# Performance work log

Measured on AMD Instinct MI355X. Metric: run time of the kernel, lower is better.

The kernel has to match this reference:

```python
import jax, jax.numpy as jnp
import numpy as np

TOP_K = 4
NORM_TOPK_PROB = True


def setup_inputs() -> dict:
    key = jax.random.key(0)
    kx, kg, k1, k3, k2 = jax.random.split(key, 5)
    B, S, H, I, E = 1, 2048, 1024, 512, 16
    scale = 0.02
    return {
        "hidden_states": jax.random.normal(kx, (B, S, H), jnp.float32),
        "gate_w": jax.random.normal(kg, (E, H), jnp.float32) * scale,   # router Linear weight [E,H]
        "w1": jax.random.normal(k1, (E, I, H), jnp.float32) * scale,    # intermediateDense per expert
        "w3": jax.random.normal(k3, (E, I, H), jnp.float32) * scale,    # intermediateDense2 per expert
        "w2": jax.random.normal(k2, (E, H, I), jnp.float32) * scale,    # outputDense per expert
    }


def reference(hidden_states, gate_w, w1, w3, w2):
    B, S, H = hidden_states.shape
    x = hidden_states.reshape(-1, H)                    # [T,H]
    T = x.shape[0]
    E = gate_w.shape[0]

    # Router: softmax in fp32, top-k, optional renorm (norm_topk_prob=True)
    router_logits = x @ gate_w.T                        # [T,E]
    probs = jax.nn.softmax(router_logits.astype(jnp.float32), axis=-1)
    routing_weights, selected = jax.lax.top_k(probs, TOP_K)   # [T,K], [T,K]
    if NORM_TOPK_PROB:
        routing_weights = routing_weights / routing_weights.sum(-1, keepdims=True)
    routing_weights = routing_weights.astype(x.dtype)

    # Dense per-token expert-weight matrix: zero for unselected experts, so
    # the combine below computes exactly the torch gather->FFN->index_add math.
    w = jnp.zeros((T, E), x.dtype).at[jnp.arange(T)[:, None], selected].add(routing_weights)

    # Gated SiLU FFN for every expert, combined with routing weights.
    h1 = jnp.einsum('th,eih->tei', x, w1)               # [T,E,I]
    h3 = jnp.einsum('th,eih->tei', x, w3)               # [T,E,I]
    act = jax.nn.silu(h1) * h3                          # [T,E,I]
    out = jnp.einsum('tei,ehi,te->th', act, w2, w)      # [T,H]
    return out.reshape(B, S, H)
```

## Files before the change

### kernel.cpp

```cpp
#include <hip/hip_runtime.h>
#include <hip/hip_bf16.h>

#define T 2048
#define H 1024
#define IDIM 512
#define E 16
#define TOPK 4
#define NPAIR (T * TOPK)

typedef short bf16x8 __attribute__((ext_vector_type(8)));
typedef float f32x4 __attribute__((ext_vector_type(4)));
typedef unsigned short u16x8 __attribute__((ext_vector_type(8)));

static __device__ __forceinline__ unsigned short f2bf(float f) {
    union { float f; unsigned int u; } v; v.f = f;
    unsigned int r = (v.u + 0x7FFFu + ((v.u >> 16) & 1u)) >> 16;
    return (unsigned short)r;
}
static __device__ __forceinline__ float bf2f(unsigned short s) {
    union { unsigned int u; float f; } v; v.u = ((unsigned int)s) << 16;
    return v.f;
}

static __device__ __forceinline__ void async_ld16(const unsigned short* g, unsigned short* l) {
    __builtin_amdgcn_global_load_lds((const __attribute__((address_space(1))) void*)g,
                                     (__attribute__((address_space(3))) void*)l, 16, 0, 0);
}

__global__ __launch_bounds__(256) void cvt3_kernel(
    const float* __restrict__ w1, const float* __restrict__ w3, const float* __restrict__ w2,
    unsigned short* __restrict__ d1, unsigned short* __restrict__ d3, unsigned short* __restrict__ d2)
{
    const int n8 = (E * IDIM * H) / 8;
    int region = blockIdx.x >> 11;
    int bid = blockIdx.x & 2047;
    const float* src = (region == 0) ? w1 : (region == 1) ? w3 : w2;
    unsigned short* dst = (region == 0) ? d1 : (region == 1) ? d3 : d2;
    int i = bid * 256 + threadIdx.x;
    const int stride = 2048 * 256;
#pragma unroll 2
    for (; i < n8; i += stride) {
        float4 a = ((const float4*)src)[2 * i];
        float4 b = ((const float4*)src)[2 * i + 1];
        u16x8 o;
        o[0] = f2bf(a.x); o[1] = f2bf(a.y); o[2] = f2bf(a.z); o[3] = f2bf(a.w);
        o[4] = f2bf(b.x); o[5] = f2bf(b.y); o[6] = f2bf(b.z); o[7] = f2bf(b.w);
        ((u16x8*)dst)[i] = o;
    }
}

__global__ __launch_bounds__(256) void router_kernel(
    const float* __restrict__ x, const float* __restrict__ gw,
    int* __restrict__ topk_idx, float* __restrict__ topk_w,
    unsigned short* __restrict__ xb)
{
    int tok = blockIdx.x * 4 + (threadIdx.x >> 6);
    int lane = threadIdx.x & 63;
    if (tok >= T) return;
    const float4* xt4 = (const float4*)(x + (size_t)tok * H);
    float4 xr[4];
#pragma unroll
    for (int j = 0; j < 4; ++j) xr[j] = xt4[lane + j * 64];
    ushort4* xbt = (ushort4*)(xb + (size_t)tok * H);
#pragma unroll
    for (int j = 0; j < 4; ++j) {
        ushort4 o;
        o.x = f2bf(xr[j].x); o.y = f2bf(xr[j].y);
        o.z = f2bf(xr[j].z); o.w = f2bf(xr[j].w);
        xbt[lane + j * 64] = o;
    }
    float logits[E];
#pragma unroll
    for (int e = 0; e < E; ++e) {
        const float4* ge4 = (const float4*)(gw + (size_t)e * H);
        float acc = 0.f;
#pragma unroll
        for (int j = 0; j < 4; ++j) {
            float4 g = ge4[lane + j * 64];
            acc += xr[j].x * g.x + xr[j].y * g.y + xr[j].z * g.z + xr[j].w * g.w;
        }
#pragma unroll
        for (int off = 32; off; off >>= 1) acc += __shfl_xor(acc, off, 64);
        logits[e] = acc;
    }
    if (lane == 0) {
        float m = logits[0];
#pragma unroll
        for (int e = 1; e < E; ++e) m = fmaxf(m, logits[e]);
        float p[E];
#pragma unroll
        for (int e = 0; e < E; ++e) p[e] = __expf(logits[e] - m);
        int sel[TOPK]; float wv[TOPK]; float tot = 0.f;
#pragma unroll
        for (int k = 0; k < TOPK; ++k) {
            int best = 0; float bv = -1.f;
#pragma unroll
            for (int e = 0; e < E; ++e) { if (p[e] > bv) { bv = p[e]; best = e; } }
            sel[k] = best; wv[k] = bv; tot += bv; p[best] = -2.f;
        }
#pragma unroll
        for (int k = 0; k < TOPK; ++k) {
            topk_idx[tok * TOPK + k] = sel[k];
            topk_w[tok * TOPK + k] = wv[k] / tot;
        }
    }
}

__global__ __launch_bounds__(1024) void route_build_kernel(
    const int* __restrict__ topk_idx, int* __restrict__ offsets,
    int* __restrict__ pair_token, int* __restrict__ inv_pos)
{
    __shared__ int h[E];
    __shared__ int cur[E];
    int tid = threadIdx.x;
    if (tid < E) h[tid] = 0;
    __syncthreads();
    int eloc[8];
#pragma unroll
    for (int j = 0; j < 8; ++j) {
        eloc[j] = topk_idx[tid * 8 + j];
        atomicAdd(&h[eloc[j]], 1);
    }
    __syncthreads();
    if (tid == 0) {
        int s = 0;
#pragma unroll
        for (int e = 0; e < E; ++e) { offsets[e] = s; cur[e] = s; s += h[e]; }
        offsets[E] = s;
    }
    __syncthreads();
#pragma unroll
    for (int j = 0; j < 8; ++j) {
        int i = tid * 8 + j;
        int pos = atomicAdd(&cur[eloc[j]], 1);
        pair_token[pos] = i >> 2;
        inv_pos[i] = pos;
    }
}


__global__ __launch_bounds__(256, 5) void gemm_a_kernel(
    const unsigned short* __restrict__ xb,
    const unsigned short* __restrict__ wb1,
    const unsigned short* __restrict__ wb3,
    const int* __restrict__ offsets,
    const int* __restrict__ pair_token,
    unsigned short* __restrict__ act)
{
    __shared__ unsigned short Xs[2][128 * 32];
    __shared__ unsigned short W1s[2][64 * 32];
    __shared__ unsigned short W3s[2][64 * 32];

    int bid = blockIdx.x;
    int xcd = bid & 7, s0 = bid >> 3;
    int yz = xcd * 16 + (s0 >> 4);
    int e = yz >> 3;
    int n0 = (yz & 7) * 64;
    int t0 = (s0 & 15) * 128;

    int beg = offsets[e];
    int cnt = offsets[e + 1] - beg;
    if (t0 >= cnt) return;

    int tid = threadIdx.x;
    int wave = tid >> 6, lane = tid & 63;

    const unsigned short* xg[2];
#pragma unroll
    for (int i = 0; i < 2; ++i) {
        int slot = wave * 128 + i * 64 + lane;
        int g = slot >> 3, sp = (slot & 7) ^ (g & 7);
        int row = g * 2 + (sp >> 2), c = sp & 3;
        int r = t0 + row; if (r >= cnt) r = cnt - 1;
        xg[i] = xb + (size_t)pair_token[beg + r] * H + c * 8;
    }
    const unsigned short* w1g;
    const unsigned short* w3g;
    {
        int slot = wave * 64 + lane;
        int g = slot >> 3, sp = (slot & 7) ^ (g & 7);
        int row = g * 2 + (sp >> 2), c = sp & 3;
        size_t off = (size_t)e * IDIM * H + (size_t)(n0 + row) * H + c * 8;
        w1g = wb1 + off;
        w3g = wb3 + off;
    }

    int wr = wave >> 1, wc = wave & 1;
    int lm = lane & 15, lq = lane >> 4;

    f32x4 acc1[4][2], acc3[4][2];
#pragma unroll
    for (int mi = 0; mi < 4; ++mi)
#pragma unroll
        for (int nj = 0; nj < 2; ++nj) {
            acc1[mi][nj] = (f32x4){0.f, 0.f, 0.f, 0.f};
            acc3[mi][nj] = (f32x4){0.f, 0.f, 0.f, 0.f};
        }

    int aoff[4], boff[2];
#pragma unroll
    for (int mi = 0; mi < 4; ++mi) {
        int m = wr * 64 + mi * 16 + lm;
        int g = m >> 1;
        aoff[mi] = g * 64 + (((lq + ((m & 1) << 2)) ^ (g & 7)) << 3);
    }
#pragma unroll
    for (int nj = 0; nj < 2; ++nj) {
        int n = wc * 32 + nj * 16 + lm;
        int g = n >> 1;
        boff[nj] = g * 64 + (((lq + ((n & 1) << 2)) ^ (g & 7)) << 3);
    }

#pragma unroll
    for (int i = 0; i < 2; ++i) async_ld16(xg[i], &Xs[0][(wave * 128 + i * 64) * 8]);
    async_ld16(w1g, &W1s[0][wave * 512]);
    async_ld16(w3g, &W3s[0][wave * 512]);

    const int NK = H / 32;
    for (int kk = 0; kk < NK; ++kk) {
        int cur = kk & 1;
        __syncthreads();
        if (kk + 1 < NK) {
            int nxt = cur ^ 1;
            int k1 = (kk + 1) * 32;
#pragma unroll
            for (int i = 0; i < 2; ++i) async_ld16(xg[i] + k1, &Xs[nxt][(wave * 128 + i * 64) * 8]);
            async_ld16(w1g + k1, &W1s[nxt][wave * 512]);
            async_ld16(w3g + k1, &W3s[nxt][wave * 512]);
        }
        bf16x8 af[4], b1[2], b3[2];
#pragma unroll
        for (int mi = 0; mi < 4; ++mi) af[mi] = *(const bf16x8*)&Xs[cur][aoff[mi]];
#pragma unroll
        for (int nj = 0; nj < 2; ++nj) {
            b1[nj] = *(const bf16x8*)&W1s[cur][boff[nj]];
            b3[nj] = *(const bf16x8*)&W3s[cur][boff[nj]];
        }
#pragma unroll
        for (int mi = 0; mi < 4; ++mi)
#pragma unroll
            for (int nj = 0; nj < 2; ++nj) {
                acc1[mi][nj] = __builtin_amdgcn_mfma_f32_16x16x32_bf16(af[mi], b1[nj], acc1[mi][nj], 0, 0, 0);
                acc3[mi][nj] = __builtin_amdgcn_mfma_f32_16x16x32_bf16(af[mi], b3[nj], acc3[mi][nj], 0, 0, 0);
            }
    }
#pragma unroll
    for (int mi = 0; mi < 4; ++mi) {
#pragma unroll
        for (int r = 0; r < 4; ++r) {
            int trow = t0 + wr * 64 + mi * 16 + lq * 4 + r;
            if (trow < cnt) {
                size_t base = (size_t)(beg + trow) * IDIM + n0 + wc * 32 + lm;
#pragma unroll
                for (int nj = 0; nj < 2; ++nj) {
                    float h1 = acc1[mi][nj][r];
                    float sg = h1 / (1.f + __expf(-h1));
                    act[base + nj * 16] = f2bf(sg * acc3[mi][nj][r]);
                }
            }
        }
    }
}

__global__ __launch_bounds__(256, 5) void gemm_b_kernel(
    const unsigned short* __restrict__ act,
    const unsigned short* __restrict__ wb2,
    const int* __restrict__ offsets,
    unsigned short* __restrict__ outp)
{
    __shared__ unsigned short As[2][128 * 32];
    __shared__ unsigned short W2s[2][64 * 32];

    int bid = blockIdx.x;
    int xcd = bid & 7, s0 = bid >> 3;
    int yz = xcd * 32 + (s0 >> 4);
    int e = yz >> 4;
    int h0 = (yz & 15) * 64;
    int t0 = (s0 & 15) * 128;

    int beg = offsets[e];
    int cnt = offsets[e + 1] - beg;
    if (t0 >= cnt) return;

    int tid = threadIdx.x;
    int wave = tid >> 6, lane = tid & 63;

    const unsigned short* ag[2];
#pragma unroll
    for (int i = 0; i < 2; ++i) {
        int slot = wave * 128 + i * 64 + lane;
        int g = slot >> 3, sp = (slot & 7) ^ (g & 7);
        int row = g * 2 + (sp >> 2), c = sp & 3;
        int ar = beg + t0 + row; if (ar > NPAIR - 1) ar = NPAIR - 1;
        ag[i] = act + (size_t)ar * IDIM + c * 8;
    }
    const unsigned short* w2g;
    {
        int slot = wave * 64 + lane;
        int g = slot >> 3, sp = (slot & 7) ^ (g & 7);
        int row = g * 2 + (sp >> 2), c = sp & 3;
        w2g = wb2 + (size_t)e * H * IDIM + (size_t)(h0 + row) * IDIM + c * 8;
    }

    int wr = wave >> 1, wc = wave & 1;
    int lm = lane & 15, lq = lane >> 4;

    f32x4 acc[4][2];
#pragma unroll
    for (int mi = 0; mi < 4; ++mi)
#pragma unroll
        for (int nj = 0; nj < 2; ++nj) acc[mi][nj] = (f32x4){0.f, 0.f, 0.f, 0.f};

    int aoff[4], boff[2];
#pragma unroll
    for (int mi = 0; mi < 4; ++mi) {
        int m = wr * 64 + mi * 16 + lm;
        int g = m >> 1;
        aoff[mi] = g * 64 + (((lq + ((m & 1) << 2)) ^ (g & 7)) << 3);
    }
#pragma unroll
    for (int nj = 0; nj < 2; ++nj) {
        int n = wc * 32 + nj * 16 + lm;
        int g = n >> 1;
        boff[nj] = g * 64 + (((lq + ((n & 1) << 2)) ^ (g & 7)) << 3);
    }

#pragma unroll
    for (int i = 0; i < 2; ++i) async_ld16(ag[i], &As[0][(wave * 128 + i * 64) * 8]);
    async_ld16(w2g, &W2s[0][wave * 512]);

    const int NK = IDIM / 32;
    for (int kk = 0; kk < NK; ++kk) {
        int cur = kk & 1;
        __syncthreads();
        if (kk + 1 < NK) {
            int nxt = cur ^ 1;
            int k1 = (kk + 1) * 32;
#pragma unroll
            for (int i = 0; i < 2; ++i) async_ld16(ag[i] + k1, &As[nxt][(wave * 128 + i * 64) * 8]);
            async_ld16(w2g + k1, &W2s[nxt][wave * 512]);
        }
        bf16x8 af[4], bfr[2];
#pragma unroll
        for (int mi = 0; mi < 4; ++mi) af[mi] = *(const bf16x8*)&As[cur][aoff[mi]];
#pragma unroll
        for (int nj = 0; nj < 2; ++nj) bfr[nj] = *(const bf16x8*)&W2s[cur][boff[nj]];
#pragma unroll
        for (int mi = 0; mi < 4; ++mi)
#pragma unroll
            for (int nj = 0; nj < 2; ++nj)
                acc[mi][nj] = __builtin_amdgcn_mfma_f32_16x16x32_bf16(af[mi], bfr[nj], acc[mi][nj], 0, 0, 0);
    }
#pragma unroll
    for (int mi = 0; mi < 4; ++mi) {
#pragma unroll
        for (int r = 0; r < 4; ++r) {
            int trow = t0 + wr * 64 + mi * 16 + lq * 4 + r;
            if (trow < cnt) {
                unsigned short* orow = outp + (size_t)(beg + trow) * H + h0 + wc * 32 + lm;
#pragma unroll
                for (int nj = 0; nj < 2; ++nj) orow[nj * 16] = f2bf(acc[mi][nj][r]);
            }
        }
    }
}

__global__ __launch_bounds__(256) void combine_kernel(
    const unsigned short* __restrict__ outp, const int* __restrict__ inv_pos,
    const float* __restrict__ topk_w, float* __restrict__ out)
{
    int gid = blockIdx.x * 256 + threadIdx.x;
    int t = gid >> 8;
    int c4 = gid & 255;
    float4 a = make_float4(0.f, 0.f, 0.f, 0.f);
#pragma unroll
    for (int k = 0; k < TOPK; ++k) {
        int pos = inv_pos[t * TOPK + k];
        float w = topk_w[t * TOPK + k];
        ushort4 v = ((const ushort4*)(outp + (size_t)pos * H))[c4];
        a.x += w * bf2f(v.x); a.y += w * bf2f(v.y);
        a.z += w * bf2f(v.z); a.w += w * bf2f(v.w);
    }
    *(float4*)(out + (size_t)t * H + c4 * 4) = a;
}

extern "C" void kernel_launch(void* const* d_in, const int* in_sizes, int n_in,
                              void* d_out, int out_size, void* d_ws, size_t ws_size,
                              hipStream_t stream)
{
    const float* x  = (const float*)d_in[0];
    const float* gw = (const float*)d_in[1];
    const float* w1 = (const float*)d_in[2];
    const float* w3 = (const float*)d_in[3];
    const float* w2 = (const float*)d_in[4];
    float* out = (float*)d_out;

    char* ws = (char*)d_ws;
    int*   offsets    = (int*)(ws + 128);
    int*   topk_idx   = (int*)(ws + 1024);
    float* topk_w     = (float*)(ws + 33792);
    int*   pair_token = (int*)(ws + 66560);
    int*   inv_pos    = (int*)(ws + 99328);
    unsigned short* xb  = (unsigned short*)(ws + 262144);
    unsigned short* wb1 = (unsigned short*)(ws + 8388608);
    unsigned short* wb3 = (unsigned short*)(ws + 25165824);
    unsigned short* wb2 = (unsigned short*)(ws + 41943040);
    unsigned short* act = (unsigned short*)(ws + 58720256);
    unsigned short* outp = (unsigned short*)(ws + 8388608);

    router_kernel<<<T / 4, 256, 0, stream>>>(x, gw, topk_idx, topk_w, xb);
    route_build_kernel<<<1, 1024, 0, stream>>>(topk_idx, offsets, pair_token, inv_pos);

    cvt3_kernel<<<3 * 2048, 256, 0, stream>>>(w1, w3, w2, wb1, wb3, wb2);

    gemm_a_kernel<<<2048, 256, 0, stream>>>(xb, wb1, wb3, offsets, pair_token, act);
    gemm_b_kernel<<<4096, 256, 0, stream>>>(act, wb2, offsets, outp);
    combine_kernel<<<(T * H / 4) / 256, 256, 0, stream>>>(outp, inv_pos, topk_w, out);
}
```

Baseline: 220.4 us.

## Fuse router, route build and weight conversion into one prep kernel

Merges the router, the single-block route build and the fp32-to-bf16 weight conversion into one launch. Router blocks come first, and the last router block to finish, found with an atomic counter plus threadfences, builds the expert offsets and permutation. This removes two kernel launches and the serialized single-block build step, and lets the routing work overlap with the bandwidth-bound weight conversion. It adds a memset launch and a last-block-done pattern, and the routing build now runs with 256 threads instead of 1024.

Measured after the change: 236.5 us. 7.3% more time.

```diff
diff --git a/kernel.cpp b/kernel.cpp
--- a/kernel.cpp
+++ b/kernel.cpp
@@ -7,6 +7,7 @@
 #define E 16
 #define TOPK 4
 #define NPAIR (T * TOPK)
+#define NRTR (T / 4)
 
 typedef short bf16x8 __attribute__((ext_vector_type(8)));
 typedef float f32x4 __attribute__((ext_vector_type(4)));
@@ -27,115 +28,124 @@
                                      (__attribute__((address_space(3))) void*)l, 16, 0, 0);
 }
 
-__global__ __launch_bounds__(256) void cvt3_kernel(
-    const float* __restrict__ w1, const float* __restrict__ w3, const float* __restrict__ w2,
-    unsigned short* __restrict__ d1, unsigned short* __restrict__ d3, unsigned short* __restrict__ d2)
-{
-    const int n8 = (E * IDIM * H) / 8;
-    int region = blockIdx.x >> 11;
-    int bid = blockIdx.x & 2047;
-    const float* src = (region == 0) ? w1 : (region == 1) ? w3 : w2;
-    unsigned short* dst = (region == 0) ? d1 : (region == 1) ? d3 : d2;
-    int i = bid * 256 + threadIdx.x;
-    const int stride = 2048 * 256;
-#pragma unroll 2
-    for (; i < n8; i += stride) {
-        float4 a = ((const float4*)src)[2 * i];
-        float4 b = ((const float4*)src)[2 * i + 1];
-        u16x8 o;
-        o[0] = f2bf(a.x); o[1] = f2bf(a.y); o[2] = f2bf(a.z); o[3] = f2bf(a.w);
-        o[4] = f2bf(b.x); o[5] = f2bf(b.y); o[6] = f2bf(b.z); o[7] = f2bf(b.w);
-        ((u16x8*)dst)[i] = o;
-    }
-}
-
-__global__ __launch_bounds__(256) void router_kernel(
+__global__ __launch_bounds__(256) void prep_kernel(
     const float* __restrict__ x, const float* __restrict__ gw,
     int* __restrict__ topk_idx, float* __restrict__ topk_w,
-    unsigned short* __restrict__ xb)
-{
-    int tok = blockIdx.x * 4 + (threadIdx.x >> 6);
-    int lane = threadIdx.x & 63;
-    if (tok >= T) return;
-    const float4* xt4 = (const float4*)(x + (size_t)tok * H);
-    float4 xr[4];
-#pragma unroll
-    for (int j = 0; j < 4; ++j) xr[j] = xt4[lane + j * 64];
-    ushort4* xbt = (ushort4*)(xb + (size_t)tok * H);
-#pragma unroll
-    for (int j = 0; j < 4; ++j) {
-        ushort4 o;
-        o.x = f2bf(xr[j].x); o.y = f2bf(xr[j].y);
-        o.z = f2bf(xr[j].z); o.w = f2bf(xr[j].w);
-        xbt[lane + j * 64] = o;
-    }
-    float logits[E];
-#pragma unroll
-    for (int e = 0; e < E; ++e) {
-        const float4* ge4 = (const float4*)(gw + (size_t)e * H);
-        float acc = 0.f;
-#pragma unroll
-        for (int j = 0; j < 4; ++j) {
-            float4 g = ge4[lane + j * 64];
-            acc += xr[j].x * g.x + xr[j].y * g.y + xr[j].z * g.z + xr[j].w * g.w;
-        }
-#pragma unroll
-        for (int off = 32; off; off >>= 1) acc += __shfl_xor(acc, off, 64);
-        logits[e] = acc;
-    }
-    if (lane == 0) {
-        float m = logits[0];
-#pragma unroll
-        for (int e = 1; e < E; ++e) m = fmaxf(m, logits[e]);
-        float p[E];
-#pragma unroll
-        for (int e = 0; e < E; ++e) p[e] = __expf(logits[e] - m);
-        int sel[TOPK]; float wv[TOPK]; float tot = 0.f;
-#pragma unroll
-        for (int k = 0; k < TOPK; ++k) {
-            int best = 0; float bv = -1.f;
-#pragma unroll
-            for (int e = 0; e < E; ++e) { if (p[e] > bv) { bv = p[e]; best = e; } }
-            sel[k] = best; wv[k] = bv; tot += bv; p[best] = -2.f;
-        }
-#pragma unroll
-        for (int k = 0; k < TOPK; ++k) {
-            topk_idx[tok * TOPK + k] = sel[k];
-            topk_w[tok * TOPK + k] = wv[k] / tot;
-        }
-    }
-}
-
-__global__ __launch_bounds__(1024) void route_build_kernel(
-    const int* __restrict__ topk_idx, int* __restrict__ offsets,
+    unsigned short* __restrict__ xb,
+    const float* __restrict__ w1, const float* __restrict__ w3, const float* __restrict__ w2,
+    unsigned short* __restrict__ d1, unsigned short* __restrict__ d3, unsigned short* __restrict__ d2,
+    int* __restrict__ done, int* __restrict__ offsets,
     int* __restrict__ pair_token, int* __restrict__ inv_pos)
 {
+    int tid = threadIdx.x;
+    if (blockIdx.x >= NRTR) {
+        const int n8 = (E * IDIM * H) / 8;
+        int cb = blockIdx.x - NRTR;
+        int region = cb >> 11;
+        int bid = cb & 2047;
+        const float* src = (region == 0) ? w1 : (region == 1) ? w3 : w2;
+        unsigned short* dst = (region == 0) ? d1 : (region == 1) ? d3 : d2;
+        int i = bid * 256 + tid;
+        const int stride = 2048 * 256;
+#pragma unroll 2
+        for (; i < n8; i += stride) {
+            float4 a = ((const float4*)src)[2 * i];
+            float4 b = ((const float4*)src)[2 * i + 1];
+            u16x8 o;
+            o[0] = f2bf(a.x); o[1] = f2bf(a.y); o[2] = f2bf(a.z); o[3] = f2bf(a.w);
+            o[4] = f2bf(b.x); o[5] = f2bf(b.y); o[6] = f2bf(b.z); o[7] = f2bf(b.w);
+            ((u16x8*)dst)[i] = o;
+        }
+        return;
+    }
+
+    int tok = blockIdx.x * 4 + (tid >> 6);
+    int lane = tid & 63;
+    {
+        const float4* xt4 = (const float4*)(x + (size_t)tok * H);
+        float4 xr[4];
+#pragma unroll
+        for (int j = 0; j < 4; ++j) xr[j] = xt4[lane + j * 64];
+        ushort4* xbt = (ushort4*)(xb + (size_t)tok * H);
+#pragma unroll
+        for (int j = 0; j < 4; ++j) {
+            ushort4 o;
+            o.x = f2bf(xr[j].x); o.y = f2bf(xr[j].y);
+            o.z = f2bf(xr[j].z); o.w = f2bf(xr[j].w);
+            xbt[lane + j * 64] = o;
+        }
+        float logits[E];
+#pragma unroll
+        for (int e = 0; e < E; ++e) {
+            const float4* ge4 = (const float4*)(gw + (size_t)e * H);
+            float acc = 0.f;
+#pragma unroll
+            for (int j = 0; j < 4; ++j) {
+                float4 g = ge4[lane + j * 64];
+                acc += xr[j].x * g.x + xr[j].y * g.y + xr[j].z * g.z + xr[j].w * g.w;
+            }
+#pragma unroll
+            for (int off = 32; off; off >>= 1) acc += __shfl_xor(acc, off, 64);
+            logits[e] = acc;
+        }
+        if (lane == 0) {
+            float m = logits[0];
+#pragma unroll
+            for (int e = 1; e < E; ++e) m = fmaxf(m, logits[e]);
+            float p[E];
+#pragma unroll
+            for (int e = 0; e < E; ++e) p[e] = __expf(logits[e] - m);
+            int sel[TOPK]; float wv[TOPK]; float tot = 0.f;
+#pragma unroll
+            for (int k = 0; k < TOPK; ++k) {
+                int best = 0; float bv = -1.f;
+#pragma unroll
+                for (int e = 0; e < E; ++e) { if (p[e] > bv) { bv = p[e]; best = e; } }
+                sel[k] = best; wv[k] = bv; tot += bv; p[best] = -2.f;
+            }
+#pragma unroll
+            for (int k = 0; k < TOPK; ++k) {
+                topk_idx[tok * TOPK + k] = sel[k];
+                topk_w[tok * TOPK + k] = wv[k] / tot;
+            }
+        }
+    }
+
+    __shared__ int flag;
     __shared__ int h[E];
-    __shared__ int cur[E];
-    int tid = threadIdx.x;
+    __shared__ int curs[E];
+    __syncthreads();
+    if (tid == 0) {
+        __threadfence();
+        flag = atomicAdd(done, 1);
+    }
+    __syncthreads();
+    if (flag != NRTR - 1) return;
+    __threadfence();
     if (tid < E) h[tid] = 0;
     __syncthreads();
-    int eloc[8];
-#pragma unroll
-    for (int j = 0; j < 8; ++j) {
-        eloc[j] = topk_idx[tid * 8 + j];
+    int eloc[NPAIR / 256];
+#pragma unroll
+    for (int j = 0; j < NPAIR / 256; ++j) {
+        eloc[j] = topk_idx[j * 256 + tid];
         atomicAdd(&h[eloc[j]], 1);
     }
     __syncthreads();
     if (tid == 0) {
         int s = 0;
 #pragma unroll
-        for (int e = 0; e < E; ++e) { offsets[e] = s; cur[e] = s; s += h[e]; }
+        for (int e = 0; e < E; ++e) { offsets[e] = s; curs[e] = s; s += h[e]; }
         offsets[E] = s;
     }
     __syncthreads();
 #pragma unroll
-    for (int j = 0; j < 8; ++j) {
-        int i = tid * 8 + j;
-        int pos = atomicAdd(&cur[eloc[j]], 1);
+    for (int j = 0; j < NPAIR / 256; ++j) {
+        int i = j * 256 + tid;
+        int pos = atomicAdd(&curs[eloc[j]], 1);
         pair_token[pos] = i >> 2;
         inv_pos[i] = pos;
     }
+    if (tid == 0) atomicExch(done, 0);
 }
 
 
@@ -396,6 +406,7 @@
     float* out = (float*)d_out;
 
     char* ws = (char*)d_ws;
+    int*   done       = (int*)(ws + 0);
     int*   offsets    = (int*)(ws + 128);
     int*   topk_idx   = (int*)(ws + 1024);
     float* topk_w     = (float*)(ws + 33792);
@@ -408,10 +419,12 @@
     unsigned short* act = (unsigned short*)(ws + 58720256);
     unsigned short* outp = (unsigned short*)(ws + 8388608);
 
-    router_kernel<<<T / 4, 256, 0, stream>>>(x, gw, topk_idx, topk_w, xb);
-    route_build_kernel<<<1, 1024, 0, stream>>>(topk_idx, offsets, pair_token, inv_pos);
-
-    cvt3_kernel<<<3 * 2048, 256, 0, stream>>>(w1, w3, w2, wb1, wb3, wb2);
+    hipMemsetAsync(ws, 0, 64, stream);
+
+    prep_kernel<<<NRTR + 3 * 2048, 256, 0, stream>>>(
+        x, gw, topk_idx, topk_w, xb,
+        w1, w3, w2, wb1, wb3, wb2,
+        done, offsets, pair_token, inv_pos);
 
     gemm_a_kernel<<<2048, 256, 0, stream>>>(xb, wb1, wb3, offsets, pair_token, act);
     gemm_b_kernel<<<4096, 256, 0, stream>>>(act, wb2, offsets, outp);
```

## Fuse routing build into gemm_a via per-block redundant histogram and scan

Applied to the files above, without the earlier changes.

Removes the single-block route_build kernel launch and folds the expert histogram, prefix scan, and token-list construction into each gemm_a block. Every block redundantly scans all top-k indices in shared memory, computes stable ranks, and builds its own 128-row token list. The designated blocks with n0==0 write inv_pos, and block (n0==0,t0==0) writes the global offsets. This removes one serial launch and the pair_token global array, but adds redundant scan work and extra barriers to all 2048 gemm_a blocks.

Result: slower. 231.0 us (+4.8%).

```diff
diff --git a/kernel.cpp b/kernel.cpp
--- a/kernel.cpp
+++ b/kernel.cpp
@@ -106,64 +106,117 @@
     }
 }
 
-__global__ __launch_bounds__(1024) void route_build_kernel(
-    const int* __restrict__ topk_idx, int* __restrict__ offsets,
-    int* __restrict__ pair_token, int* __restrict__ inv_pos)
-{
-    __shared__ int h[E];
-    __shared__ int cur[E];
-    int tid = threadIdx.x;
-    if (tid < E) h[tid] = 0;
-    __syncthreads();
-    int eloc[8];
-#pragma unroll
-    for (int j = 0; j < 8; ++j) {
-        eloc[j] = topk_idx[tid * 8 + j];
-        atomicAdd(&h[eloc[j]], 1);
-    }
-    __syncthreads();
-    if (tid == 0) {
-        int s = 0;
-#pragma unroll
-        for (int e = 0; e < E; ++e) { offsets[e] = s; cur[e] = s; s += h[e]; }
-        offsets[E] = s;
-    }
-    __syncthreads();
-#pragma unroll
-    for (int j = 0; j < 8; ++j) {
-        int i = tid * 8 + j;
-        int pos = atomicAdd(&cur[eloc[j]], 1);
-        pair_token[pos] = i >> 2;
-        inv_pos[i] = pos;
-    }
-}
-
 
 __global__ __launch_bounds__(256, 5) void gemm_a_kernel(
     const unsigned short* __restrict__ xb,
     const unsigned short* __restrict__ wb1,
     const unsigned short* __restrict__ wb3,
-    const int* __restrict__ offsets,
-    const int* __restrict__ pair_token,
+    const int* __restrict__ topk_idx,
+    int* __restrict__ offsets,
+    int* __restrict__ inv_pos,
     unsigned short* __restrict__ act)
 {
-    __shared__ unsigned short Xs[2][128 * 32];
-    __shared__ unsigned short W1s[2][64 * 32];
-    __shared__ unsigned short W3s[2][64 * 32];
+    __shared__ unsigned char SM[32768];
+    unsigned short* Xs  = (unsigned short*)SM;
+    unsigned short* W1s = (unsigned short*)(SM + 16384);
+    unsigned short* W3s = (unsigned short*)(SM + 24576);
+    unsigned char*  eb     = SM;
+    unsigned short* c2d    = (unsigned short*)(SM + 8192);
+    int*            offs_l = (int*)(SM + 16448);
+    unsigned short* tokw   = (unsigned short*)(SM + 16520);
 
     int bid = blockIdx.x;
     int xcd = bid & 7, s0 = bid >> 3;
     int yz = xcd * 16 + (s0 >> 4);
-    int e = yz >> 3;
+    int eB = yz >> 3;
     int n0 = (yz & 7) * 64;
     int t0 = (s0 & 15) * 128;
 
-    int beg = offsets[e];
-    int cnt = offsets[e + 1] - beg;
-    if (t0 >= cnt) return;
-
     int tid = threadIdx.x;
     int wave = tid >> 6, lane = tid & 63;
+
+    unsigned long long lcA = 0, lcB = 0;
+    {
+        const int4* tsrc = (const int4*)(topk_idx + tid * 32);
+#pragma unroll
+        for (int q = 0; q < 8; ++q) {
+            int4 v = tsrc[q];
+            ((unsigned int*)eb)[tid * 8 + q] =
+                (unsigned)v.x | ((unsigned)v.y << 8) | ((unsigned)v.z << 16) | ((unsigned)v.w << 24);
+#pragma unroll
+            for (int c = 0; c < 4; ++c) {
+                int ee = (c == 0) ? v.x : (c == 1) ? v.y : (c == 2) ? v.z : v.w;
+                unsigned long long inc = 1ull << ((ee & 7) * 8);
+                lcA += (ee < 8) ? inc : 0ull;
+                lcB += (ee < 8) ? 0ull : inc;
+            }
+        }
+    }
+#pragma unroll
+    for (int ee = 0; ee < 8; ++ee) {
+        c2d[(tid + 1) * 16 + ee]     = (unsigned short)((lcA >> (ee * 8)) & 0xff);
+        c2d[(tid + 1) * 16 + 8 + ee] = (unsigned short)((lcB >> (ee * 8)) & 0xff);
+    }
+    __syncthreads();
+    if (tid < 16) {
+        int run = 0;
+        for (int q = 1; q <= 256; ++q) {
+            int v = c2d[q * 16 + tid];
+            c2d[q * 16 + tid] = (unsigned short)run;
+            run += v;
+        }
+        c2d[tid] = (unsigned short)run;
+    }
+    __syncthreads();
+    if (tid == 0) {
+        int s = 0;
+#pragma unroll
+        for (int ee = 0; ee < E; ++ee) { offs_l[ee] = s; s += c2d[ee]; }
+        offs_l[E] = s;
+    }
+    __syncthreads();
+    int beg = offs_l[eB];
+    int cnt = offs_l[eB + 1] - beg;
+    if (n0 == 0 && t0 == 0 && tid < 17) offsets[tid] = offs_l[tid];
+    if (t0 >= cnt) return;
+
+    {
+        int b_ = (tid + 1) * 16;
+        unsigned long long r0 = (unsigned long long)c2d[b_ + 0] | ((unsigned long long)c2d[b_ + 1] << 16)
+                              | ((unsigned long long)c2d[b_ + 2] << 32) | ((unsigned long long)c2d[b_ + 3] << 48);
+        unsigned long long r1 = (unsigned long long)c2d[b_ + 4] | ((unsigned long long)c2d[b_ + 5] << 16)
+                              | ((unsigned long long)c2d[b_ + 6] << 32) | ((unsigned long long)c2d[b_ + 7] << 48);
+        unsigned long long r2 = (unsigned long long)c2d[b_ + 8] | ((unsigned long long)c2d[b_ + 9] << 16)
+                              | ((unsigned long long)c2d[b_ + 10] << 32) | ((unsigned long long)c2d[b_ + 11] << 48);
+        unsigned long long r3 = (unsigned long long)c2d[b_ + 12] | ((unsigned long long)c2d[b_ + 13] << 16)
+                              | ((unsigned long long)c2d[b_ + 14] << 32) | ((unsigned long long)c2d[b_ + 15] << 48);
+        bool wr_inv = (n0 == 0);
+#pragma unroll
+        for (int q = 0; q < 8; ++q) {
+            unsigned int pk = ((unsigned int*)eb)[tid * 8 + q];
+#pragma unroll
+            for (int c = 0; c < 4; ++c) {
+                int ee = (pk >> (c * 8)) & 0xff;
+                int grp = ee >> 2, sh = (ee & 3) * 16;
+                unsigned long long cur = (grp == 0) ? r0 : (grp == 1) ? r1 : (grp == 2) ? r2 : r3;
+                int rk = (int)((cur >> sh) & 0xffffull);
+                unsigned long long inc = 1ull << sh;
+                r0 += (grp == 0) ? inc : 0ull;
+                r1 += (grp == 1) ? inc : 0ull;
+                r2 += (grp == 2) ? inc : 0ull;
+                r3 += (grp == 3) ? inc : 0ull;
+                if (ee == eB) {
+                    unsigned int w = (unsigned)(rk - t0);
+                    if (w < 128u) {
+                        int i = tid * 32 + q * 4 + c;
+                        tokw[w] = (unsigned short)(i >> 2);
+                        if (wr_inv) inv_pos[i] = beg + rk;
+                    }
+                }
+            }
+        }
+    }
+    __syncthreads();
 
     const unsigned short* xg[2];
 #pragma unroll
@@ -171,8 +224,8 @@
         int slot = wave * 128 + i * 64 + lane;
         int g = slot >> 3, sp = (slot & 7) ^ (g & 7);
         int row = g * 2 + (sp >> 2), c = sp & 3;
-        int r = t0 + row; if (r >= cnt) r = cnt - 1;
-        xg[i] = xb + (size_t)pair_token[beg + r] * H + c * 8;
+        int rr = t0 + row; if (rr >= cnt) rr = cnt - 1;
+        xg[i] = xb + (size_t)tokw[rr - t0] * H + c * 8;
     }
     const unsigned short* w1g;
     const unsigned short* w3g;
@@ -180,10 +233,11 @@
         int slot = wave * 64 + lane;
         int g = slot >> 3, sp = (slot & 7) ^ (g & 7);
         int row = g * 2 + (sp >> 2), c = sp & 3;
-        size_t off = (size_t)e * IDIM * H + (size_t)(n0 + row) * H + c * 8;
+        size_t off = (size_t)eB * IDIM * H + (size_t)(n0 + row) * H + c * 8;
         w1g = wb1 + off;
         w3g = wb3 + off;
     }
+    __syncthreads();
 
     int wr = wave >> 1, wc = wave & 1;
     int lm = lane & 15, lq = lane >> 4;
@@ -212,9 +266,9 @@
     }
 
 #pragma unroll
-    for (int i = 0; i < 2; ++i) async_ld16(xg[i], &Xs[0][(wave * 128 + i * 64) * 8]);
-    async_ld16(w1g, &W1s[0][wave * 512]);
-    async_ld16(w3g, &W3s[0][wave * 512]);
+    for (int i = 0; i < 2; ++i) async_ld16(xg[i], Xs + (wave * 128 + i * 64) * 8);
+    async_ld16(w1g, W1s + wave * 512);
+    async_ld16(w3g, W3s + wave * 512);
 
     const int NK = H / 32;
     for (int kk = 0; kk < NK; ++kk) {
@@ -224,17 +278,18 @@
             int nxt = cur ^ 1;
             int k1 = (kk + 1) * 32;
 #pragma unroll
-            for (int i = 0; i < 2; ++i) async_ld16(xg[i] + k1, &Xs[nxt][(wave * 128 + i * 64) * 8]);
-            async_ld16(w1g + k1, &W1s[nxt][wave * 512]);
-            async_ld16(w3g + k1, &W3s[nxt][wave * 512]);
+            for (int i = 0; i < 2; ++i)
+                async_ld16(xg[i] + k1, Xs + nxt * 4096 + (wave * 128 + i * 64) * 8);
+            async_ld16(w1g + k1, W1s + nxt * 2048 + wave * 512);
+            async_ld16(w3g + k1, W3s + nxt * 2048 + wave * 512);
         }
         bf16x8 af[4], b1[2], b3[2];
 #pragma unroll
-        for (int mi = 0; mi < 4; ++mi) af[mi] = *(const bf16x8*)&Xs[cur][aoff[mi]];
+        for (int mi = 0; mi < 4; ++mi) af[mi] = *(const bf16x8*)(Xs + cur * 4096 + aoff[mi]);
 #pragma unroll
         for (int nj = 0; nj < 2; ++nj) {
-            b1[nj] = *(const bf16x8*)&W1s[cur][boff[nj]];
-            b3[nj] = *(const bf16x8*)&W3s[cur][boff[nj]];
+            b1[nj] = *(const bf16x8*)(W1s + cur * 2048 + boff[nj]);
+            b3[nj] = *(const bf16x8*)(W3s + cur * 2048 + boff[nj]);
         }
 #pragma unroll
         for (int mi = 0; mi < 4; ++mi)
@@ -399,7 +454,6 @@
     int*   offsets    = (int*)(ws + 128);
     int*   topk_idx   = (int*)(ws + 1024);
     float* topk_w     = (float*)(ws + 33792);
-    int*   pair_token = (int*)(ws + 66560);
     int*   inv_pos    = (int*)(ws + 99328);
     unsigned short* xb  = (unsigned short*)(ws + 262144);
     unsigned short* wb1 = (unsigned short*)(ws + 8388608);
@@ -409,11 +463,9 @@
     unsigned short* outp = (unsigned short*)(ws + 8388608);
 
     router_kernel<<<T / 4, 256, 0, stream>>>(x, gw, topk_idx, topk_w, xb);
-    route_build_kernel<<<1, 1024, 0, stream>>>(topk_idx, offsets, pair_token, inv_pos);
-
     cvt3_kernel<<<3 * 2048, 256, 0, stream>>>(w1, w3, w2, wb1, wb3, wb2);
 
-    gemm_a_kernel<<<2048, 256, 0, stream>>>(xb, wb1, wb3, offsets, pair_token, act);
+    gemm_a_kernel<<<2048, 256, 0, stream>>>(xb, wb1, wb3, topk_idx, offsets, inv_pos, act);
     gemm_b_kernel<<<4096, 256, 0, stream>>>(act, wb2, offsets, outp);
     combine_kernel<<<(T * H / 4) / 256, 256, 0, stream>>>(outp, inv_pos, topk_w, out);
 }
```

## Fuse weighted combine into down-projection GEMM epilogue via atomic adds

Applied to the files above, without the earlier changes.

Removes the separate combine kernel and the bf16 per-pair output buffer. The down-projection GEMM now scales each row by its routing weight and atomically adds it into the fp32 output at the token's row. The output is zeroed in the router kernel. This saves one launch and the round trip through the intermediate buffer, at the cost of many scalar fp32 atomics and a nondeterministic summation order.

New measurement: 239.1 us. +8.5%, slower.

```diff
diff --git a/kernel.cpp b/kernel.cpp
--- a/kernel.cpp
+++ b/kernel.cpp
@@ -52,11 +52,17 @@
 __global__ __launch_bounds__(256) void router_kernel(
     const float* __restrict__ x, const float* __restrict__ gw,
     int* __restrict__ topk_idx, float* __restrict__ topk_w,
-    unsigned short* __restrict__ xb)
+    unsigned short* __restrict__ xb, float* __restrict__ out)
 {
     int tok = blockIdx.x * 4 + (threadIdx.x >> 6);
     int lane = threadIdx.x & 63;
     if (tok >= T) return;
+    {
+        float4 z = make_float4(0.f, 0.f, 0.f, 0.f);
+        float4* orow = (float4*)(out + (size_t)tok * H);
+#pragma unroll
+        for (int j = 0; j < 4; ++j) orow[lane + j * 64] = z;
+    }
     const float4* xt4 = (const float4*)(x + (size_t)tok * H);
     float4 xr[4];
 #pragma unroll
@@ -107,8 +113,9 @@
 }
 
 __global__ __launch_bounds__(1024) void route_build_kernel(
-    const int* __restrict__ topk_idx, int* __restrict__ offsets,
-    int* __restrict__ pair_token, int* __restrict__ inv_pos)
+    const int* __restrict__ topk_idx, const float* __restrict__ topk_w,
+    int* __restrict__ offsets,
+    int* __restrict__ pair_token, float* __restrict__ pair_w)
 {
     __shared__ int h[E];
     __shared__ int cur[E];
@@ -134,7 +141,7 @@
         int i = tid * 8 + j;
         int pos = atomicAdd(&cur[eloc[j]], 1);
         pair_token[pos] = i >> 2;
-        inv_pos[i] = pos;
+        pair_w[pos] = topk_w[i];
     }
 }
 
@@ -266,7 +273,9 @@
     const unsigned short* __restrict__ act,
     const unsigned short* __restrict__ wb2,
     const int* __restrict__ offsets,
-    unsigned short* __restrict__ outp)
+    const int* __restrict__ pair_token,
+    const float* __restrict__ pair_w,
+    float* __restrict__ out)
 {
     __shared__ unsigned short As[2][128 * 32];
     __shared__ unsigned short W2s[2][64 * 32];
@@ -357,31 +366,15 @@
         for (int r = 0; r < 4; ++r) {
             int trow = t0 + wr * 64 + mi * 16 + lq * 4 + r;
             if (trow < cnt) {
-                unsigned short* orow = outp + (size_t)(beg + trow) * H + h0 + wc * 32 + lm;
-#pragma unroll
-                for (int nj = 0; nj < 2; ++nj) orow[nj * 16] = f2bf(acc[mi][nj][r]);
+                int p = beg + trow;
+                int tok = pair_token[p];
+                float wgt = pair_w[p];
+                float* orow = out + (size_t)tok * H + h0 + wc * 32 + lm;
+                atomicAdd(&orow[0],  wgt * acc[mi][0][r]);
+                atomicAdd(&orow[16], wgt * acc[mi][1][r]);
             }
         }
     }
-}
-
-__global__ __launch_bounds__(256) void combine_kernel(
-    const unsigned short* __restrict__ outp, const int* __restrict__ inv_pos,
-    const float* __restrict__ topk_w, float* __restrict__ out)
-{
-    int gid = blockIdx.x * 256 + threadIdx.x;
-    int t = gid >> 8;
-    int c4 = gid & 255;
-    float4 a = make_float4(0.f, 0.f, 0.f, 0.f);
-#pragma unroll
-    for (int k = 0; k < TOPK; ++k) {
-        int pos = inv_pos[t * TOPK + k];
-        float w = topk_w[t * TOPK + k];
-        ushort4 v = ((const ushort4*)(outp + (size_t)pos * H))[c4];
-        a.x += w * bf2f(v.x); a.y += w * bf2f(v.y);
-        a.z += w * bf2f(v.z); a.w += w * bf2f(v.w);
-    }
-    *(float4*)(out + (size_t)t * H + c4 * 4) = a;
 }
 
 extern "C" void kernel_launch(void* const* d_in, const int* in_sizes, int n_in,
@@ -400,20 +393,18 @@
     int*   topk_idx   = (int*)(ws + 1024);
     float* topk_w     = (float*)(ws + 33792);
     int*   pair_token = (int*)(ws + 66560);
-    int*   inv_pos    = (int*)(ws + 99328);
+    float* pair_w     = (float*)(ws + 99328);
     unsigned short* xb  = (unsigned short*)(ws + 262144);
     unsigned short* wb1 = (unsigned short*)(ws + 8388608);
     unsigned short* wb3 = (unsigned short*)(ws + 25165824);
     unsigned short* wb2 = (unsigned short*)(ws + 41943040);
     unsigned short* act = (unsigned short*)(ws + 58720256);
-    unsigned short* outp = (unsigned short*)(ws + 8388608);
-
-    router_kernel<<<T / 4, 256, 0, stream>>>(x, gw, topk_idx, topk_w, xb);
-    route_build_kernel<<<1, 1024, 0, stream>>>(topk_idx, offsets, pair_token, inv_pos);
+
+    router_kernel<<<T / 4, 256, 0, stream>>>(x, gw, topk_idx, topk_w, xb, out);
+    route_build_kernel<<<1, 1024, 0, stream>>>(topk_idx, topk_w, offsets, pair_token, pair_w);
 
     cvt3_kernel<<<3 * 2048, 256, 0, stream>>>(w1, w3, w2, wb1, wb3, wb2);
 
     gemm_a_kernel<<<2048, 256, 0, stream>>>(xb, wb1, wb3, offsets, pair_token, act);
-    gemm_b_kernel<<<4096, 256, 0, stream>>>(act, wb2, offsets, outp);
-    combine_kernel<<<(T * H / 4) / 256, 256, 0, stream>>>(outp, inv_pos, topk_w, out);
-}
+    gemm_b_kernel<<<4096, 256, 0, stream>>>(act, wb2, offsets, pair_token, pair_w, out);
+}
```
